# Kernel tuning notes

Measured on AMD Instinct MI355X. Metric: run time of the kernel, lower is better.

## Reference

```python
import jax, jax.numpy as jnp
import numpy as np


def _next_pow2(n: int) -> int:
    return 1 << (max(int(n), 1) - 1).bit_length()


def setup_inputs() -> dict:
    key = jax.random.key(0)
    k1, k2 = jax.random.split(key)
    B, L, D, K = 8, 8192, 256, 8192
    u = jax.random.normal(k1, (B, L, D), dtype=jnp.float32)
    h = jax.random.normal(k2, (D, K), dtype=jnp.float32) * 0.02  # RandomNormal(stddev=0.02)
    return {"u": u, "h": h}


def reference(u, h):
    # Depthwise long conv via zero-padded FFT, 'same' padding.
    # Faithful to the TF code, including its h-row pairing via tf.repeat:
    # x row i (= b*D + d) is multiplied by filter row i // B.
    u = u.astype(jnp.float32)
    B, L, D = u.shape
    K = h.shape[1]
    N = _next_pow2(L + K - 1)

    x = jnp.transpose(u, (0, 2, 1)).reshape(B * D, L)      # (B*D, L)
    x_pad = jnp.pad(x, ((0, 0), (0, N - L)))               # (B*D, N)
    h_pad = jnp.pad(h, ((0, 0), (0, N - K)))               # (D, N)

    X = jnp.fft.rfft(x_pad, axis=-1)                       # (B*D, N//2+1)
    H = jnp.fft.rfft(h_pad, axis=-1)                       # (D, N//2+1)
    # tf.repeat(h, B, axis=0): repeated row i corresponds to filter i // B
    row_filter = jnp.arange(B * D) // B                    # (B*D,)
    Y = X * H[row_filter]

    y_full = jnp.fft.irfft(Y, n=N, axis=-1)                # (B*D, N)
    start = (K - 1) // 2
    y = y_full[:, start:start + L]                         # (B*D, L)
    y = y.reshape(B, D, L)
    return jnp.transpose(y, (0, 2, 1))                     # (B, L, D)
```

## Files before the change

kernel.cpp:

```cpp
#include <hip/hip_runtime.h>

#define TPB 1024

__device__ constexpr int PX(int p) { return p + 2 * (p >> 5); }

#define LDS_F2 17408
#define LDS_BYTES (LDS_F2 * 8)

template<int S, bool INV>
__device__ __forceinline__ void fft_stage(float2* __restrict__ A, int tid) {
  constexpr int LG = (S==4096)?12:(S==1024)?10:(S==256)?8:(S==64)?6:(S==16)?4:(S==4)?2:0;
  const int np = tid & (S - 1);
  const int base0 = ((tid >> LG) << (LG + 2)) | np;
  float2* P = A + PX(base0);
  const float tws = (INV ? 1.5707963267948966f : -1.5707963267948966f) / (float)S;
  float c1, s1;
  if (S == 1) { c1 = 1.f; s1 = 0.f; } else { __sincosf(tws * (float)np, &s1, &c1); }
  float c2 = c1*c1 - s1*s1, s2 = 2.f*c1*s1;
  float c3 = c1*c2 - s1*s2, s3 = c1*s2 + s1*c2;
  __syncthreads();
#pragma unroll
  for (int m = 0; m < 4; ++m) {
    if (S == 4096 && m) {
      constexpr float WC = 0.92387953251128674f;
      const float WS = INV ? 0.38268343236508978f : -0.38268343236508978f;
      float t = c1*WC - s1*WS; s1 = c1*WS + s1*WC; c1 = t;
      c2 = c1*c1 - s1*s1; s2 = 2.f*c1*s1;
      c3 = c1*c2 - s1*s2; s3 = c1*s2 + s1*c2;
    }
    const int mo = (S == 4096) ? 1024 * m : 4096 * m;
    const int o0 = PX(mo);
    const int o1 = PX(mo + S);
    const int o2 = PX(mo + 2*S);
    const int o3 = PX(mo + 3*S);
    if (!INV) {
      float2 a = P[o0], b = P[o1], c = P[o2], d = P[o3];
      float t0r = a.x + c.x, t0i = a.y + c.y;
      float t1r = a.x - c.x, t1i = a.y - c.y;
      float t2r = b.x + d.x, t2i = b.y + d.y;
      float t3r = b.x - d.x, t3i = b.y - d.y;
      float u0r = t0r + t2r, u0i = t0i + t2i;
      float u2r = t0r - t2r, u2i = t0i - t2i;
      float u1r = t1r + t3i, u1i = t1i - t3r;
      float u3r = t1r - t3i, u3i = t1i + t3r;
      P[o0] = make_float2(u0r, u0i);
      P[o1] = make_float2(u1r*c1 - u1i*s1, u1r*s1 + u1i*c1);
      P[o2] = make_float2(u2r*c2 - u2i*s2, u2r*s2 + u2i*c2);
      P[o3] = make_float2(u3r*c3 - u3i*s3, u3r*s3 + u3i*c3);
    } else {
      float2 v0 = P[o0], u1 = P[o1], u2 = P[o2], u3 = P[o3];
      float v1r = u1.x*c1 - u1.y*s1, v1i = u1.x*s1 + u1.y*c1;
      float v2r = u2.x*c2 - u2.y*s2, v2i = u2.x*s2 + u2.y*c2;
      float v3r = u3.x*c3 - u3.y*s3, v3i = u3.x*s3 + u3.y*c3;
      P[o0] = make_float2(v0.x + v1r + v2r + v3r, v0.y + v1i + v2i + v3i);
      P[o1] = make_float2(v0.x - v1i - v2r + v3i, v0.y + v1r - v2i - v3r);
      P[o2] = make_float2(v0.x - v1r + v2r - v3r, v0.y - v1i + v2i - v3i);
      P[o3] = make_float2(v0.x + v1i - v2r - v3i, v0.y - v1r - v2i + v3r);
    }
  }
}

__device__ __forceinline__ void fft_fwd(float2* A, int tid) {
  fft_stage<4096,false>(A,tid); fft_stage<1024,false>(A,tid);
  fft_stage<256,false>(A,tid);  fft_stage<64,false>(A,tid);
  fft_stage<16,false>(A,tid);   fft_stage<4,false>(A,tid);
  fft_stage<1,false>(A,tid);
}
__device__ __forceinline__ void fft_inv(float2* A, int tid) {
  fft_stage<1,true>(A,tid);    fft_stage<4,true>(A,tid);
  fft_stage<16,true>(A,tid);   fft_stage<64,true>(A,tid);
  fft_stage<256,true>(A,tid);  fft_stage<1024,true>(A,tid);
  fft_stage<4096,true>(A,tid);
}

__global__ __launch_bounds__(TPB) void h_fft(const float* __restrict__ h,
                                             float2* __restrict__ Hbuf) {
  extern __shared__ __align__(16) float2 A[];
  const int tid = threadIdx.x;
  const int f = blockIdx.x;
  const float4* h4 = (const float4*)(h + (size_t)f * 8192);
#pragma unroll
  for (int m = 0; m < 2; ++m) {
    int g = tid + TPB * m;
    float4 a = h4[g];
    int p = 4 * g;
    *(float4*)&A[PX(p)]     = make_float4(a.x, 0.f, a.y, 0.f);
    *(float4*)&A[PX(p) + 2] = make_float4(a.z, 0.f, a.w, 0.f);
    int z = p + 8192;
    *(float4*)&A[PX(z)]     = make_float4(0.f, 0.f, 0.f, 0.f);
    *(float4*)&A[PX(z) + 2] = make_float4(0.f, 0.f, 0.f, 0.f);
  }
  fft_fwd(A, tid);
  __syncthreads();
  float2* orow = Hbuf + (size_t)f * 16384;
  const float sc = 1.f / 16384.f;
#pragma unroll
  for (int m = 0; m < 8; ++m) {
    int p = 2 * (tid + TPB * m);
    float4 za = *(const float4*)&A[PX(p)];
    *(float4*)&orow[p] = make_float4(za.x * sc, za.y * sc, za.z * sc, za.w * sc);
  }
}

__global__ void transpose_in(const float* __restrict__ u, float* __restrict__ xT) {
  __shared__ float4 T[64 * 16];
  const int l0 = blockIdx.x * 64, d0 = blockIdx.y * 64, b = blockIdx.z;
  const int t = threadIdx.x, c = t & 15, r = t >> 4;
  const float4* u4 = (const float4*)(u + (size_t)b * 8192 * 256);
  float* Tf = (float*)T;
#pragma unroll
  for (int p = 0; p < 4; ++p) {
    int li = r + 16 * p;
    float4 v = u4[(size_t)(l0 + li) * 64 + (d0 >> 2) + c];
    int lc = li >> 2, lk = li & 3;
#pragma unroll
    for (int k = 0; k < 4; ++k) {
      int dr = 4 * c + k;
      Tf[(dr * 16 + (lc ^ (dr & 15))) * 4 + lk] = ((const float*)&v)[k];
    }
  }
  __syncthreads();
#pragma unroll
  for (int p = 0; p < 4; ++p) {
    int dr = r + 16 * p;
    float4 w = T[dr * 16 + (c ^ (dr & 15))];
    *(float4*)&xT[(size_t)(b * 256 + d0 + dr) * 8192 + l0 + 4 * c] = w;
  }
}

__global__ void transpose_out(const float* __restrict__ yT, float* __restrict__ out) {
  __shared__ float4 T[64 * 16];
  const int l0 = blockIdx.x * 64, d0 = blockIdx.y * 64, b = blockIdx.z;
  const int t = threadIdx.x, c = t & 15, r = t >> 4;
  float* Tf = (float*)T;
#pragma unroll
  for (int p = 0; p < 4; ++p) {
    int di = r + 16 * p;
    float4 v = *(const float4*)&yT[(size_t)(b * 256 + d0 + di) * 8192 + l0 + 4 * c];
    int dc = di >> 2, dk = di & 3;
#pragma unroll
    for (int k = 0; k < 4; ++k) {
      int lr = 4 * c + k;
      Tf[(lr * 16 + (dc ^ (lr & 15))) * 4 + dk] = ((const float*)&v)[k];
    }
  }
  __syncthreads();
#pragma unroll
  for (int p = 0; p < 4; ++p) {
    int lr = r + 16 * p;
    float4 w = T[lr * 16 + (c ^ (lr & 15))];
    *(float4*)&out[(size_t)(b * 8192 + l0 + lr) * 256 + d0 + 4 * c] = w;
  }
}

__global__ __launch_bounds__(TPB) void conv_main(const float* __restrict__ xT,
                                                 const float2* __restrict__ Hbuf,
                                                 float* yT) {
  extern __shared__ __align__(16) float2 A[];
  const int tid = threadIdx.x;
  const int i = blockIdx.x;
  const int f = ((i >> 5) << 3) | (i & 7);
  const int r = (f << 3) | (((i >> 3) & 3) << 1);
  const float4* xr0 = (const float4*)(xT + (size_t)r * 8192);
  const float4* xr1 = (const float4*)(xT + (size_t)(r + 1) * 8192);
#pragma unroll
  for (int m = 0; m < 2; ++m) {
    int g = tid + TPB * m;
    float4 a = xr0[g];
    float4 b = xr1[g];
    int p = 4 * g;
    *(float4*)&A[PX(p)]     = make_float4(a.x, b.x, a.y, b.y);
    *(float4*)&A[PX(p) + 2] = make_float4(a.z, b.z, a.w, b.w);
    int z = p + 8192;
    *(float4*)&A[PX(z)]     = make_float4(0.f, 0.f, 0.f, 0.f);
    *(float4*)&A[PX(z) + 2] = make_float4(0.f, 0.f, 0.f, 0.f);
  }
  fft_fwd(A, tid);
  __syncthreads();
  const float2* Hrow = Hbuf + (size_t)f * 16384;
#pragma unroll
  for (int m = 0; m < 8; ++m) {
    int p = 2 * (tid + TPB * m);
    float4 za = *(const float4*)&A[PX(p)];
    float4 hv = *(const float4*)&Hrow[p];
    *(float4*)&A[PX(p)] = make_float4(za.x*hv.x - za.y*hv.y, za.x*hv.y + za.y*hv.x,
                                      za.z*hv.z - za.w*hv.w, za.z*hv.w + za.w*hv.z);
  }
  fft_inv(A, tid);
  __syncthreads();
  float* y0 = yT + (size_t)r * 8192;
  float* y1 = yT + (size_t)(r + 1) * 8192;
#pragma unroll
  for (int m = 0; m < 8; ++m) {
    int l = tid + TPB * m;
    float2 w = A[PX(l + 4095)];
    y0[l] = w.x;
    y1[l] = w.y;
  }
}

extern "C" void kernel_launch(void* const* d_in, const int* in_sizes, int n_in,
                              void* d_out, int out_size, void* d_ws, size_t ws_size,
                              hipStream_t stream) {
  (void)in_sizes; (void)n_in; (void)out_size; (void)ws_size;
  const float* u = (const float*)d_in[0];
  const float* h = (const float*)d_in[1];
  float* out = (float*)d_out;
  float* xT = (float*)d_ws;
  float2* Hbuf = (float2*)((char*)d_ws + (size_t)2048 * 8192 * 4);

  static_assert(LDS_BYTES == 139264, "lds");
  (void)hipFuncSetAttribute((const void*)h_fft,
      hipFuncAttributeMaxDynamicSharedMemorySize, LDS_BYTES);
  (void)hipFuncSetAttribute((const void*)conv_main,
      hipFuncAttributeMaxDynamicSharedMemorySize, LDS_BYTES);

  h_fft<<<256, TPB, LDS_BYTES, stream>>>(h, Hbuf);
  transpose_in<<<dim3(128, 4, 8), 256, 0, stream>>>(u, xT);
  conv_main<<<1024, TPB, LDS_BYTES, stream>>>(xT, Hbuf, xT);
  transpose_out<<<dim3(128, 4, 8), 256, 0, stream>>>(xT, out);
}
```

Measured before the change: 277.6 us.

## Restructure FFT as register-resident radix-16 passes with fused first/last stages

Replaces the seven radix-4 LDS passes with radix-16 butterflies held in registers, so each forward and inverse FFT needs about three LDS round trips and barriers instead of seven. The first radix-16 pass reads global memory directly and exploits the zero-padded upper half (r4dif_z). The final forward radix-4 stage, the pointwise multiply by H, and the first inverse radix-4 stage are fused into one register pass. The last inverse pass writes the output slice straight to global memory. This cuts LDS traffic and barriers at the cost of more registers per thread and strided global loads and stores.

Result: faster. 241.4 us (-13.0%).

```diff
diff --git a/kernel.cpp b/kernel.cpp
--- a/kernel.cpp
+++ b/kernel.cpp
@@ -7,70 +7,129 @@
 #define LDS_F2 17408
 #define LDS_BYTES (LDS_F2 * 8)
 
-template<int S, bool INV>
-__device__ __forceinline__ void fft_stage(float2* __restrict__ A, int tid) {
-  constexpr int LG = (S==4096)?12:(S==1024)?10:(S==256)?8:(S==64)?6:(S==16)?4:(S==4)?2:0;
-  const int np = tid & (S - 1);
-  const int base0 = ((tid >> LG) << (LG + 2)) | np;
-  float2* P = A + PX(base0);
-  const float tws = (INV ? 1.5707963267948966f : -1.5707963267948966f) / (float)S;
-  float c1, s1;
-  if (S == 1) { c1 = 1.f; s1 = 0.f; } else { __sincosf(tws * (float)np, &s1, &c1); }
-  float c2 = c1*c1 - s1*s1, s2 = 2.f*c1*s1;
-  float c3 = c1*c2 - s1*s2, s3 = c1*s2 + s1*c2;
-  __syncthreads();
-#pragma unroll
-  for (int m = 0; m < 4; ++m) {
-    if (S == 4096 && m) {
-      constexpr float WC = 0.92387953251128674f;
-      const float WS = INV ? 0.38268343236508978f : -0.38268343236508978f;
-      float t = c1*WC - s1*WS; s1 = c1*WS + s1*WC; c1 = t;
-      c2 = c1*c1 - s1*s1; s2 = 2.f*c1*s1;
-      c3 = c1*c2 - s1*s2; s3 = c1*s2 + s1*c2;
-    }
-    const int mo = (S == 4096) ? 1024 * m : 4096 * m;
-    const int o0 = PX(mo);
-    const int o1 = PX(mo + S);
-    const int o2 = PX(mo + 2*S);
-    const int o3 = PX(mo + 3*S);
-    if (!INV) {
-      float2 a = P[o0], b = P[o1], c = P[o2], d = P[o3];
-      float t0r = a.x + c.x, t0i = a.y + c.y;
-      float t1r = a.x - c.x, t1i = a.y - c.y;
-      float t2r = b.x + d.x, t2i = b.y + d.y;
-      float t3r = b.x - d.x, t3i = b.y - d.y;
-      float u0r = t0r + t2r, u0i = t0i + t2i;
-      float u2r = t0r - t2r, u2i = t0i - t2i;
-      float u1r = t1r + t3i, u1i = t1i - t3r;
-      float u3r = t1r - t3i, u3i = t1i + t3r;
-      P[o0] = make_float2(u0r, u0i);
-      P[o1] = make_float2(u1r*c1 - u1i*s1, u1r*s1 + u1i*c1);
-      P[o2] = make_float2(u2r*c2 - u2i*s2, u2r*s2 + u2i*c2);
-      P[o3] = make_float2(u3r*c3 - u3i*s3, u3r*s3 + u3i*c3);
-    } else {
-      float2 v0 = P[o0], u1 = P[o1], u2 = P[o2], u3 = P[o3];
-      float v1r = u1.x*c1 - u1.y*s1, v1i = u1.x*s1 + u1.y*c1;
-      float v2r = u2.x*c2 - u2.y*s2, v2i = u2.x*s2 + u2.y*c2;
-      float v3r = u3.x*c3 - u3.y*s3, v3i = u3.x*s3 + u3.y*c3;
-      P[o0] = make_float2(v0.x + v1r + v2r + v3r, v0.y + v1i + v2i + v3i);
-      P[o1] = make_float2(v0.x - v1i - v2r + v3i, v0.y + v1r - v2i - v3r);
-      P[o2] = make_float2(v0.x - v1r + v2r - v3r, v0.y - v1i + v2i - v3i);
-      P[o3] = make_float2(v0.x + v1i - v2r - v3i, v0.y - v1r - v2i + v3r);
-    }
-  }
-}
-
-__device__ __forceinline__ void fft_fwd(float2* A, int tid) {
-  fft_stage<4096,false>(A,tid); fft_stage<1024,false>(A,tid);
-  fft_stage<256,false>(A,tid);  fft_stage<64,false>(A,tid);
-  fft_stage<16,false>(A,tid);   fft_stage<4,false>(A,tid);
-  fft_stage<1,false>(A,tid);
-}
-__device__ __forceinline__ void fft_inv(float2* A, int tid) {
-  fft_stage<1,true>(A,tid);    fft_stage<4,true>(A,tid);
-  fft_stage<16,true>(A,tid);   fft_stage<64,true>(A,tid);
-  fft_stage<256,true>(A,tid);  fft_stage<1024,true>(A,tid);
-  fft_stage<4096,true>(A,tid);
+#define PIF 3.14159265358979323846f
+#define C8 0.92387953251128674f
+#define S8 0.38268343236508978f
+
+struct Tw { float c1,s1,c2,s2,c3,s3; };
+
+__device__ __forceinline__ Tw tw_make(float c1, float s1) {
+  Tw w;
+  w.c1 = c1; w.s1 = s1;
+  w.c2 = c1*c1 - s1*s1;      w.s2 = 2.f*c1*s1;
+  w.c3 = c1*w.c2 - s1*w.s2;  w.s3 = c1*w.s2 + s1*w.c2;
+  return w;
+}
+__device__ __forceinline__ Tw tw_angle(float a) {
+  float s, c; __sincosf(a, &s, &c); return tw_make(c, s);
+}
+
+__device__ __forceinline__ void r4dif(float2&a,float2&b,float2&c,float2&d,const Tw&w){
+  float t0r=a.x+c.x, t0i=a.y+c.y, t1r=a.x-c.x, t1i=a.y-c.y;
+  float t2r=b.x+d.x, t2i=b.y+d.y, t3r=b.x-d.x, t3i=b.y-d.y;
+  float u0r=t0r+t2r, u0i=t0i+t2i, u2r=t0r-t2r, u2i=t0i-t2i;
+  float u1r=t1r+t3i, u1i=t1i-t3r, u3r=t1r-t3i, u3i=t1i+t3r;
+  a = make_float2(u0r, u0i);
+  b = make_float2(u1r*w.c1 - u1i*w.s1, u1r*w.s1 + u1i*w.c1);
+  c = make_float2(u2r*w.c2 - u2i*w.s2, u2r*w.s2 + u2i*w.c2);
+  d = make_float2(u3r*w.c3 - u3i*w.s3, u3r*w.s3 + u3i*w.c3);
+}
+__device__ __forceinline__ void r4dif_z(float2&a,float2&b,float2&c,float2&d,const Tw&w){
+  float u0r=a.x+b.x, u0i=a.y+b.y, u2r=a.x-b.x, u2i=a.y-b.y;
+  float u1r=a.x+b.y, u1i=a.y-b.x, u3r=a.x-b.y, u3i=a.y+b.x;
+  a = make_float2(u0r, u0i);
+  b = make_float2(u1r*w.c1 - u1i*w.s1, u1r*w.s1 + u1i*w.c1);
+  c = make_float2(u2r*w.c2 - u2i*w.s2, u2r*w.s2 + u2i*w.c2);
+  d = make_float2(u3r*w.c3 - u3i*w.s3, u3r*w.s3 + u3i*w.c3);
+}
+__device__ __forceinline__ void r4dif_nt(float2&a,float2&b,float2&c,float2&d){
+  float t0r=a.x+c.x, t0i=a.y+c.y, t1r=a.x-c.x, t1i=a.y-c.y;
+  float t2r=b.x+d.x, t2i=b.y+d.y, t3r=b.x-d.x, t3i=b.y-d.y;
+  a = make_float2(t0r+t2r, t0i+t2i);
+  b = make_float2(t1r+t3i, t1i-t3r);
+  c = make_float2(t0r-t2r, t0i-t2i);
+  d = make_float2(t1r-t3i, t1i+t3r);
+}
+__device__ __forceinline__ void r4dit(float2&a,float2&b,float2&c,float2&d,const Tw&w){
+  float v1r=b.x*w.c1 - b.y*w.s1, v1i=b.x*w.s1 + b.y*w.c1;
+  float v2r=c.x*w.c2 - c.y*w.s2, v2i=c.x*w.s2 + c.y*w.c2;
+  float v3r=d.x*w.c3 - d.y*w.s3, v3i=d.x*w.s3 + d.y*w.c3;
+  float ar=a.x, ai=a.y;
+  a = make_float2(ar+v1r+v2r+v3r, ai+v1i+v2i+v3i);
+  b = make_float2(ar-v1i-v2r+v3i, ai+v1r-v2i-v3r);
+  c = make_float2(ar-v1r+v2r-v3r, ai-v1i+v2i-v3i);
+  d = make_float2(ar+v1i-v2r-v3i, ai-v1r-v2i+v3r);
+}
+__device__ __forceinline__ void r4dit_nt(float2&a,float2&b,float2&c,float2&d){
+  float v1r=b.x, v1i=b.y, v2r=c.x, v2i=c.y, v3r=d.x, v3i=d.y;
+  float ar=a.x, ai=a.y;
+  a = make_float2(ar+v1r+v2r+v3r, ai+v1i+v2i+v3i);
+  b = make_float2(ar-v1i-v2r+v3i, ai+v1r-v2i-v3r);
+  c = make_float2(ar-v1r+v2r-v3r, ai-v1i+v2i-v3i);
+  d = make_float2(ar+v1i-v2r-v3i, ai-v1r-v2i+v3r);
+}
+
+__device__ __forceinline__ void r16_fwd(float2 (&e)[16], float aA, float aB) {
+  float c1, s1; __sincosf(aA, &s1, &c1);
+#pragma unroll
+  for (int r = 0; r < 4; ++r) {
+    if (r) { float t = c1*C8 + s1*S8; s1 = s1*C8 - c1*S8; c1 = t; }
+    Tw w = tw_make(c1, s1);
+    r4dif(e[r], e[r+4], e[r+8], e[r+12], w);
+  }
+  Tw wb = tw_angle(aB);
+#pragma unroll
+  for (int m = 0; m < 4; ++m) r4dif(e[4*m], e[4*m+1], e[4*m+2], e[4*m+3], wb);
+}
+__device__ __forceinline__ void r16_fwd_z(float2 (&e)[16], float aA, float aB) {
+  float c1, s1; __sincosf(aA, &s1, &c1);
+#pragma unroll
+  for (int r = 0; r < 4; ++r) {
+    if (r) { float t = c1*C8 + s1*S8; s1 = s1*C8 - c1*S8; c1 = t; }
+    Tw w = tw_make(c1, s1);
+    r4dif_z(e[r], e[r+4], e[r+8], e[r+12], w);
+  }
+  Tw wb = tw_angle(aB);
+#pragma unroll
+  for (int m = 0; m < 4; ++m) r4dif(e[4*m], e[4*m+1], e[4*m+2], e[4*m+3], wb);
+}
+__device__ __forceinline__ void r16_inv(float2 (&e)[16], float aA, float aB) {
+  Tw wa = tw_angle(aA);
+#pragma unroll
+  for (int j = 0; j < 4; ++j) r4dit(e[4*j], e[4*j+1], e[4*j+2], e[4*j+3], wa);
+  float c1, s1; __sincosf(aB, &s1, &c1);
+#pragma unroll
+  for (int q = 0; q < 4; ++q) {
+    if (q) { float t = c1*C8 - s1*S8; s1 = s1*C8 + c1*S8; c1 = t; }
+    Tw w = tw_make(c1, s1);
+    r4dit(e[q], e[q+4], e[q+8], e[q+12], w);
+  }
+}
+
+__device__ __forceinline__ void fwd_mid(float2* A, int tid) {
+  __syncthreads();
+  {
+    const int c = tid & 63;
+    const int pb = PX(((tid >> 6) << 10) | c);
+    float2 e[16];
+#pragma unroll
+    for (int k = 0; k < 16; ++k) e[k] = A[pb + PX(64*k)];
+    r16_fwd(e, (float)c * (-PIF/512.f), (float)c * (-PIF/128.f));
+#pragma unroll
+    for (int k = 0; k < 16; ++k) A[pb + PX(64*k)] = e[k];
+  }
+  __syncthreads();
+  {
+    const int c = tid & 3;
+    const int pb = PX(((tid >> 2) << 6) | c);
+    float2 e[16];
+#pragma unroll
+    for (int k = 0; k < 16; ++k) e[k] = A[pb + PX(4*k)];
+    r16_fwd(e, (float)c * (-PIF/32.f), (float)c * (-PIF/8.f));
+#pragma unroll
+    for (int k = 0; k < 16; ++k) A[pb + PX(4*k)] = e[k];
+  }
+  __syncthreads();
 }
 
 __global__ __launch_bounds__(TPB) void h_fft(const float* __restrict__ h,
@@ -78,27 +137,29 @@
   extern __shared__ __align__(16) float2 A[];
   const int tid = threadIdx.x;
   const int f = blockIdx.x;
-  const float4* h4 = (const float4*)(h + (size_t)f * 8192);
-#pragma unroll
-  for (int m = 0; m < 2; ++m) {
-    int g = tid + TPB * m;
-    float4 a = h4[g];
-    int p = 4 * g;
-    *(float4*)&A[PX(p)]     = make_float4(a.x, 0.f, a.y, 0.f);
-    *(float4*)&A[PX(p) + 2] = make_float4(a.z, 0.f, a.w, 0.f);
-    int z = p + 8192;
-    *(float4*)&A[PX(z)]     = make_float4(0.f, 0.f, 0.f, 0.f);
-    *(float4*)&A[PX(z) + 2] = make_float4(0.f, 0.f, 0.f, 0.f);
-  }
-  fft_fwd(A, tid);
-  __syncthreads();
+  const float* hr = h + (size_t)f * 8192;
+  float2 e[16];
+#pragma unroll
+  for (int k = 0; k < 8; ++k) e[k] = make_float2(hr[tid + 1024*k], 0.f);
+  r16_fwd_z(e, (float)tid * (-PIF/8192.f), (float)tid * (-PIF/2048.f));
+  const int pt = PX(tid);
+#pragma unroll
+  for (int k = 0; k < 16; ++k) A[pt + PX(1024*k)] = e[k];
+  fwd_mid(A, tid);
+  const float sc = 1.f / 16384.f;
   float2* orow = Hbuf + (size_t)f * 16384;
-  const float sc = 1.f / 16384.f;
-#pragma unroll
-  for (int m = 0; m < 8; ++m) {
-    int p = 2 * (tid + TPB * m);
-    float4 za = *(const float4*)&A[PX(p)];
-    *(float4*)&orow[p] = make_float4(za.x * sc, za.y * sc, za.z * sc, za.w * sc);
+  const int p4 = PX(4*tid);
+#pragma unroll
+  for (int m = 0; m < 4; ++m) {
+    const int pp = p4 + PX(4096*m);
+    float4 lo = *(const float4*)&A[pp];
+    float4 hi = *(const float4*)&A[pp+2];
+    float2 a = make_float2(lo.x, lo.y), b = make_float2(lo.z, lo.w);
+    float2 c = make_float2(hi.x, hi.y), d = make_float2(hi.z, hi.w);
+    r4dif_nt(a, b, c, d);
+    const int p = 4*tid + 4096*m;
+    *(float4*)&orow[p]   = make_float4(a.x*sc, a.y*sc, b.x*sc, b.y*sc);
+    *(float4*)&orow[p+2] = make_float4(c.x*sc, c.y*sc, d.x*sc, d.y*sc);
   }
 }
 
@@ -161,41 +222,80 @@
   const int i = blockIdx.x;
   const int f = ((i >> 5) << 3) | (i & 7);
   const int r = (f << 3) | (((i >> 3) & 3) << 1);
-  const float4* xr0 = (const float4*)(xT + (size_t)r * 8192);
-  const float4* xr1 = (const float4*)(xT + (size_t)(r + 1) * 8192);
-#pragma unroll
-  for (int m = 0; m < 2; ++m) {
-    int g = tid + TPB * m;
-    float4 a = xr0[g];
-    float4 b = xr1[g];
-    int p = 4 * g;
-    *(float4*)&A[PX(p)]     = make_float4(a.x, b.x, a.y, b.y);
-    *(float4*)&A[PX(p) + 2] = make_float4(a.z, b.z, a.w, b.w);
-    int z = p + 8192;
-    *(float4*)&A[PX(z)]     = make_float4(0.f, 0.f, 0.f, 0.f);
-    *(float4*)&A[PX(z) + 2] = make_float4(0.f, 0.f, 0.f, 0.f);
-  }
-  fft_fwd(A, tid);
-  __syncthreads();
-  const float2* Hrow = Hbuf + (size_t)f * 16384;
-#pragma unroll
-  for (int m = 0; m < 8; ++m) {
-    int p = 2 * (tid + TPB * m);
-    float4 za = *(const float4*)&A[PX(p)];
-    float4 hv = *(const float4*)&Hrow[p];
-    *(float4*)&A[PX(p)] = make_float4(za.x*hv.x - za.y*hv.y, za.x*hv.y + za.y*hv.x,
-                                      za.z*hv.z - za.w*hv.w, za.z*hv.w + za.w*hv.z);
-  }
-  fft_inv(A, tid);
-  __syncthreads();
-  float* y0 = yT + (size_t)r * 8192;
-  float* y1 = yT + (size_t)(r + 1) * 8192;
-#pragma unroll
-  for (int m = 0; m < 8; ++m) {
-    int l = tid + TPB * m;
-    float2 w = A[PX(l + 4095)];
-    y0[l] = w.x;
-    y1[l] = w.y;
+  const float* x0 = xT + (size_t)r * 8192;
+  const float* x1 = xT + (size_t)(r + 1) * 8192;
+
+  float2 e[16];
+#pragma unroll
+  for (int k = 0; k < 8; ++k)
+    e[k] = make_float2(x0[tid + 1024*k], x1[tid + 1024*k]);
+  r16_fwd_z(e, (float)tid * (-PIF/8192.f), (float)tid * (-PIF/2048.f));
+  const int pt = PX(tid);
+#pragma unroll
+  for (int k = 0; k < 16; ++k) A[pt + PX(1024*k)] = e[k];
+
+  fwd_mid(A, tid);
+
+  {
+    const float2* Hrow = Hbuf + (size_t)f * 16384;
+    const int p4 = PX(4*tid);
+#pragma unroll
+    for (int m = 0; m < 4; ++m) {
+      const int pp = p4 + PX(4096*m);
+      float4 lo = *(const float4*)&A[pp];
+      float4 hi = *(const float4*)&A[pp+2];
+      float2 a = make_float2(lo.x, lo.y), b = make_float2(lo.z, lo.w);
+      float2 c = make_float2(hi.x, hi.y), d = make_float2(hi.z, hi.w);
+      r4dif_nt(a, b, c, d);
+      const int p = 4*tid + 4096*m;
+      float4 h0 = *(const float4*)&Hrow[p];
+      float4 h1 = *(const float4*)&Hrow[p+2];
+      float2 an = make_float2(a.x*h0.x - a.y*h0.y, a.x*h0.y + a.y*h0.x);
+      float2 bn = make_float2(b.x*h0.z - b.y*h0.w, b.x*h0.w + b.y*h0.z);
+      float2 cn = make_float2(c.x*h1.x - c.y*h1.y, c.x*h1.y + c.y*h1.x);
+      float2 dn = make_float2(d.x*h1.z - d.y*h1.w, d.x*h1.w + d.y*h1.z);
+      r4dit_nt(an, bn, cn, dn);
+      *(float4*)&A[pp]   = make_float4(an.x, an.y, bn.x, bn.y);
+      *(float4*)&A[pp+2] = make_float4(cn.x, cn.y, dn.x, dn.y);
+    }
+  }
+  __syncthreads();
+
+  {
+    const int c = tid & 3;
+    const int pb = PX(((tid >> 2) << 6) | c);
+#pragma unroll
+    for (int k = 0; k < 16; ++k) e[k] = A[pb + PX(4*k)];
+    r16_inv(e, (float)c * (PIF/8.f), (float)c * (PIF/32.f));
+#pragma unroll
+    for (int k = 0; k < 16; ++k) A[pb + PX(4*k)] = e[k];
+  }
+  __syncthreads();
+
+  {
+    const int c = tid & 63;
+    const int pb = PX(((tid >> 6) << 10) | c);
+#pragma unroll
+    for (int k = 0; k < 16; ++k) e[k] = A[pb + PX(64*k)];
+    r16_inv(e, (float)c * (PIF/128.f), (float)c * (PIF/512.f));
+#pragma unroll
+    for (int k = 0; k < 16; ++k) A[pb + PX(64*k)] = e[k];
+  }
+  __syncthreads();
+
+  {
+#pragma unroll
+    for (int k = 0; k < 16; ++k) e[k] = A[pt + PX(1024*k)];
+    r16_inv(e, (float)tid * (PIF/2048.f), (float)tid * (PIF/8192.f));
+    float* y0 = yT + (size_t)r * 8192;
+    float* y1 = yT + (size_t)(r + 1) * 8192;
+#pragma unroll
+    for (int k = 4; k <= 10; ++k) {
+      const int l = tid + 1024*k - 4095;
+      y0[l] = e[k].x; y1[l] = e[k].y;
+    }
+    if (tid < 1023) { const int l = tid + 1024*11 - 4095; y0[l] = e[11].x; y1[l] = e[11].y; }
+    else            { y0[0] = e[3].x;  y1[0] = e[3].y; }
   }
 }
 
```
